# Kernel tuning notes

Measured on AMD Instinct MI355X. Metric: run time of the kernel, lower is better.

The kernel has to match this reference:

```python
import jax, jax.numpy as jnp
import numpy as np

EPS = 1e-5
ND, NDIS, NP, NG, NPW = 40000, 40000, 80000, 80000, 40000
D = 128


def gcn(x_src, src, dst, n_dst, W, b):
    # DGL GraphConv with norm='both': D_dst^{-1/2} A^T D_src^{-1/2} X W + b
    deg_out = jnp.maximum(jnp.zeros((x_src.shape[0],), x_src.dtype).at[src].add(1.0), 1.0)
    xs = x_src * (deg_out ** -0.5)[:, None]
    msg = jax.ops.segment_sum(xs[src], dst, num_segments=n_dst)
    deg_in = jnp.maximum(jnp.zeros((n_dst,), x_src.dtype).at[dst].add(1.0), 1.0)
    return (msg * (deg_in ** -0.5)[:, None]) @ W + b


def bn_prelu(v, gamma, beta, a):
    # BatchNorm1d (training-mode batch stats, biased var) then PReLU (scalar slope)
    mu = v.mean(0)
    var = v.var(0)
    y = gamma * (v - mu) / jnp.sqrt(var + EPS) + beta
    return jnp.where(y >= 0, y, a * y)


def sem_att(z, W1, b1, w2):
    # z: [N, K, D]; shared SemanticAttention across node types
    s = jnp.tanh(z @ W1 + b1) @ w2        # [N, K]
    beta = jax.nn.softmax(s.mean(0))       # [K]
    return jnp.einsum('k,nkd->nd', beta, z)


def setup_inputs():
    key = jax.random.key(0)
    ks = iter(jax.random.split(key, 40))
    f = lambda n: jax.random.normal(next(ks), (n, D), jnp.float32)
    inp = {'h_drug': f(ND), 'h_disease': f(NDIS), 'h_protein': f(NP),
           'h_gene': f(NG), 'h_pathway': f(NPW)}
    rels = {'dd': (ND, ND, 640000), 'ddi': (ND, NDIS, 640000), 'disdis': (NDIS, NDIS, 640000),
            'dp': (ND, NP, 640000), 'pp': (NP, NP, 1280000), 'pg': (NP, NG, 1280000),
            'gg': (NG, NG, 1280000), 'gpw': (NG, NPW, 1280000), 'pwpw': (NPW, NPW, 640000),
            'pwdis': (NPW, NDIS, 640000)}
    for name, (ns, nd, E) in rels.items():
        inp[name + '_src'] = jax.random.randint(next(ks), (E,), 0, ns)
        inp[name + '_dst'] = jax.random.randint(next(ks), (E,), 0, nd)
    inp['W_blocks'] = jax.random.normal(next(ks), (5, 3, D, D), jnp.float32) * 0.09
    inp['b_blocks'] = jnp.zeros((5, 3, D), jnp.float32)
    inp['bn_gamma'] = jnp.ones((5, D), jnp.float32)
    inp['bn_beta'] = jnp.zeros((5, D), jnp.float32)
    inp['prelu_a'] = jnp.full((5,), 0.25, jnp.float32)
    inp['attn_W1'] = jax.random.normal(next(ks), (D, D), jnp.float32) * 0.09
    inp['attn_b1'] = jnp.zeros((D,), jnp.float32)
    inp['attn_w2'] = jax.random.normal(next(ks), (D,), jnp.float32) * 0.09
    return inp


def reference(h_drug, h_disease, h_protein, h_gene, h_pathway,
              dd_src, dd_dst, ddi_src, ddi_dst, disdis_src, disdis_dst,
              dp_src, dp_dst, pp_src, pp_dst, pg_src, pg_dst,
              gg_src, gg_dst, gpw_src, gpw_dst, pwpw_src, pwpw_dst,
              pwdis_src, pwdis_dst,
              W_blocks, b_blocks, bn_gamma, bn_beta, prelu_a,
              attn_W1, attn_b1, attn_w2):
    act = lambda i, v: bn_prelu(v, bn_gamma[i], bn_beta[i], prelu_a[i])
    # block 0: drug_disease  (rels: drug_drug, drug_disease, disease_disease)
    d0 = act(0, gcn(h_drug, dd_src, dd_dst, ND, W_blocks[0, 0], b_blocks[0, 0]))
    dis0 = act(0, gcn(h_drug, ddi_src, ddi_dst, NDIS, W_blocks[0, 1], b_blocks[0, 1])
               + gcn(h_disease, disdis_src, disdis_dst, NDIS, W_blocks[0, 2], b_blocks[0, 2]))
    # block 1: drug_protein
    d1 = act(1, gcn(h_drug, dd_src, dd_dst, ND, W_blocks[1, 0], b_blocks[1, 0]))
    p1 = act(1, gcn(h_drug, dp_src, dp_dst, NP, W_blocks[1, 1], b_blocks[1, 1])
             + gcn(h_protein, pp_src, pp_dst, NP, W_blocks[1, 2], b_blocks[1, 2]))
    # block 2: protein_gene
    p2 = act(2, gcn(h_protein, pp_src, pp_dst, NP, W_blocks[2, 0], b_blocks[2, 0]))
    g2 = act(2, gcn(h_protein, pg_src, pg_dst, NG, W_blocks[2, 1], b_blocks[2, 1])
             + gcn(h_gene, gg_src, gg_dst, NG, W_blocks[2, 2], b_blocks[2, 2]))
    # block 3: gene_pathway
    g3 = act(3, gcn(h_gene, gg_src, gg_dst, NG, W_blocks[3, 0], b_blocks[3, 0]))
    pw3 = act(3, gcn(h_gene, gpw_src, gpw_dst, NPW, W_blocks[3, 1], b_blocks[3, 1])
              + gcn(h_pathway, pwpw_src, pwpw_dst, NPW, W_blocks[3, 2], b_blocks[3, 2]))
    # block 4: pathway_disease
    pw4 = act(4, gcn(h_pathway, pwpw_src, pwpw_dst, NPW, W_blocks[4, 0], b_blocks[4, 0]))
    dis4 = act(4, gcn(h_pathway, pwdis_src, pwdis_dst, NDIS, W_blocks[4, 1], b_blocks[4, 1])
               + gcn(h_disease, disdis_src, disdis_dst, NDIS, W_blocks[4, 2], b_blocks[4, 2]))
    att = lambda a, b: sem_att(jnp.stack([a, b], axis=1), attn_W1, attn_b1, attn_w2)
    return (att(d0, d1), att(dis0, dis4), att(p1, p2), att(g2, g3), att(pw3, pw4))
```

## Files before the change

kernel.cpp:

```cpp
#include <hip/hip_runtime.h>
#include <hip/hip_bf16.h>

#define D128 128

typedef __attribute__((ext_vector_type(8))) short bf16x8;
typedef __attribute__((ext_vector_type(4))) float f32x4;

__device__ inline unsigned short f2bf(float f) {
    unsigned u = __float_as_uint(f);
    u = u + 0x7fffu + ((u >> 16) & 1u);
    return (unsigned short)(u >> 16);
}
__device__ inline float bf2f(unsigned short h) {
    return __uint_as_float(((unsigned)h) << 16);
}
__device__ inline float fast_tanh(float x) {
    float e = __expf(2.f * x);
    return 1.f - 2.f * __builtin_amdgcn_rcpf(e + 1.f);
}

__device__ __forceinline__ void stage_w(const unsigned short* __restrict__ Wt,
                                        unsigned short* lw, int t)
{
    const uint4* srcW = (const uint4*)Wt;
    uint4* dstW = (uint4*)lw;
    for (int i = t; i < 2048; i += 256) {
        int row = i >> 4, sl = i & 15;
        dstW[row * 16 + (sl ^ (row & 7))] = srcW[i];
    }
}
__device__ __forceinline__ bf16x8 read_w(const unsigned short* lw, int row, int kt, int lq)
{
    int slot = (kt * 4 + lq) ^ (row & 7);
    return *(const bf16x8*)(lw + row * 128 + slot * 8);
}

__global__ __launch_bounds__(256) void xconv_scaled(
    const float* __restrict__ in, const int* __restrict__ degs,
    unsigned* __restrict__ out, int nrows)
{
    int t = threadIdx.x;
    int lane = t & 63, rr = t >> 6;
    int row = blockIdx.x * 4 + rr;
    if (row >= nrows) return;
    float sc = rsqrtf((float)max(degs[row], 1));
    float2 v = ((const float2*)(in + (size_t)row * 128))[lane];
    out[(size_t)row * 64 + lane] =
        (unsigned)f2bf(v.x * sc) | ((unsigned)f2bf(v.y * sc) << 16);
}

__global__ void wconv_t(const float* __restrict__ W_blocks, const float* __restrict__ W1,
                        unsigned short* __restrict__ wt)
{
    int m = blockIdx.x;
    const float* src = (m < 15) ? (W_blocks + (size_t)m * 16384) : W1;
    unsigned short* dst = wt + (size_t)m * 16384;
    for (int i = threadIdx.x; i < 16384; i += 256) {
        int n = i >> 7, k = i & 127;
        dst[i] = f2bf(src[k * 128 + n]);
    }
}

struct BuildArgs {
    const int* esrc[10]; const int* edst[10];
    int* histD; int* histS;
    int cumBlk[11]; int dstColBase[11]; int srcColBase[11]; int E[10];
};

__global__ __launch_bounds__(256) void part_count(BuildArgs A)
{
    __shared__ int hd[160], hs[320];
    int blk = blockIdx.x, t = threadIdx.x;
    int r = 0;
    while (r < 9 && blk >= A.cumBlk[r + 1]) r++;
    int blkInRel = blk - A.cumBlk[r];
    int nbD = A.dstColBase[r + 1] - A.dstColBase[r];
    int nbS = A.srcColBase[r + 1] - A.srcColBase[r];
    for (int i = t; i < nbD; i += 256) hd[i] = 0;
    for (int i = t; i < nbS; i += 256) hs[i] = 0;
    __syncthreads();
    int e0 = blkInRel * 16384;
    const int* sp = A.esrc[r];
    const int* dp = A.edst[r];
    int E = A.E[r];
#pragma unroll 4
    for (int j = 0; j < 64; j++) {
        int e = e0 + j * 256 + t;
        if (e < E) {
            atomicAdd(&hd[dp[e] >> 9], 1);
            atomicAdd(&hs[sp[e] >> 8], 1);
        }
    }
    __syncthreads();
    int cd = A.dstColBase[r], cs = A.srcColBase[r];
    for (int i = t; i < nbD; i += 256)
        A.histD[(size_t)(cd + i) * 80 + blkInRel] = hd[i];
    for (int i = t; i < nbS; i += 256)
        A.histS[(size_t)(cs + i) * 80 + blkInRel] = hs[i];
}

struct ScanArgs { int* hist; int* totals; int colBase[11]; int cumBlk[11]; };

__global__ __launch_bounds__(256) void col_scan(ScanArgs A)
{
    __shared__ int v[80];
    int col = blockIdx.x, t = threadIdx.x;
    int r = 0;
    while (r < 9 && col >= A.colBase[r + 1]) r++;
    int nblk = A.cumBlk[r + 1] - A.cumBlk[r];
    for (int i = t; i < nblk; i += 256) v[i] = A.hist[(size_t)col * 80 + i];
    __syncthreads();
    if (t == 0) {
        int run = 0;
        for (int i = 0; i < nblk; i++) { int c = v[i]; v[i] = run; run += c; }
        A.totals[col] = run;
    }
    __syncthreads();
    for (int i = t; i < nblk; i += 256) A.hist[(size_t)col * 80 + i] = v[i];
}

__global__ __launch_bounds__(256) void base_scan(const int* __restrict__ totals,
                                                 int* __restrict__ colbase, int n)
{
    __shared__ int v[2200];
    int t = threadIdx.x;
    for (int i = t; i < n; i += 256) v[i] = totals[i];
    __syncthreads();
    if (t == 0) {
        int run = 0;
        for (int i = 0; i < n; i++) { int c = v[i]; v[i] = run; run += c; }
        v[n] = run;
    }
    __syncthreads();
    for (int i = t; i <= n; i += 256) colbase[i] = v[i];
}

struct ScatArgs {
    const int* esrc[10]; const int* edst[10];
    const int* histD; const int* colbaseD;
    const int* histS; const int* colbaseS;
    int* epart; unsigned char* spart;
    int cumBlk[11]; int dstColBase[11]; int srcColBase[11]; int E[10];
};

__global__ __launch_bounds__(256) void scatter_all(ScatArgs A)
{
    __shared__ int hd[160], based[160], hs[320], bases[320];
    int blk = blockIdx.x, t = threadIdx.x;
    int r = 0;
    while (r < 9 && blk >= A.cumBlk[r + 1]) r++;
    int blkInRel = blk - A.cumBlk[r];
    int cd = A.dstColBase[r], cs = A.srcColBase[r];
    int nbD = A.dstColBase[r + 1] - cd;
    int nbS = A.srcColBase[r + 1] - cs;
    for (int i = t; i < nbD; i += 256) {
        based[i] = A.colbaseD[cd + i] + A.histD[(size_t)(cd + i) * 80 + blkInRel];
        hd[i] = 0;
    }
    for (int i = t; i < nbS; i += 256) {
        bases[i] = A.colbaseS[cs + i] + A.histS[(size_t)(cs + i) * 80 + blkInRel];
        hs[i] = 0;
    }
    __syncthreads();
    int e0 = blkInRel * 16384;
    const int* sp = A.esrc[r];
    const int* dp = A.edst[r];
    int E = A.E[r];
#pragma unroll 4
    for (int j = 0; j < 64; j++) {
        int e = e0 + j * 256 + t;
        if (e < E) {
            int s = sp[e], d = dp[e];
            int bd = d >> 9;
            int pd = atomicAdd(&hd[bd], 1);
            A.epart[based[bd] + pd] = (s & 0x1FFFF) | ((d & 511) << 17);
            int bs = s >> 8;
            int ps = atomicAdd(&hs[bs], 1);
            A.spart[(size_t)bases[bs] + ps] = (unsigned char)(s & 255);
        }
    }
}

struct FillArgs {
    const int* epart; const int* colbase;
    int* cursor; int* ebuf; int* oflow;
    int colBase[11];
    int cursorBase[10]; int ebufBase[10]; int cap[10]; int nd[10];
};

__global__ __launch_bounds__(256) void bucket_fill(FillArgs A)
{
    __shared__ int lcur[512];
    int col = blockIdx.x, t = threadIdx.x;
    int r = 0;
    while (r < 9 && col >= A.colBase[r + 1]) r++;
    int b = col - A.colBase[r];
    for (int i = t; i < 512; i += 256) lcur[i] = 0;
    __syncthreads();
    int start = A.colbase[col], end = A.colbase[col + 1];
    int cap = A.cap[r];
    int* eb = A.ebuf + (size_t)A.ebufBase[r];
    int* ofl = A.oflow + r * 8194;
    for (int i = start + t; i < end; i += 256) {
        int v = A.epart[i];
        int s = v & 0x1FFFF;
        int dlow = (v >> 17) & 511;
        int p = atomicAdd(&lcur[dlow], 1);
        if (p < cap) eb[(size_t)(b * 512 + dlow) * cap + p] = s;
        else {
            int q = atomicAdd(&ofl[0], 1);
            if (q < 4095) { ofl[2 + 2 * q] = b * 512 + dlow; ofl[3 + 2 * q] = s; }
        }
    }
    __syncthreads();
    for (int i = t; i < 512; i += 256) {
        int d = b * 512 + i;
        if (d < A.nd[r]) A.cursor[A.cursorBase[r] + d] = lcur[i];
    }
}

struct DegArgs {
    const unsigned char* spart; const int* colbase;
    int* degs;
    int colBase[11]; int degsBase[10]; int ns[10];
};

__global__ __launch_bounds__(256) void deg_count(DegArgs A)
{
    __shared__ int lc[256];
    int col = blockIdx.x, t = threadIdx.x;
    int r = 0;
    while (r < 9 && col >= A.colBase[r + 1]) r++;
    int b = col - A.colBase[r];
    lc[t] = 0;
    __syncthreads();
    int start = A.colbase[col], end = A.colbase[col + 1];
    for (int i = start + t; i < end; i += 256)
        atomicAdd(&lc[A.spart[i]], 1);
    __syncthreads();
    int s = b * 256 + t;
    if (s < A.ns[r]) A.degs[A.degsBase[r] + s] = lc[t];
}

__global__ __launch_bounds__(256) void gather_bf16(
    const unsigned* __restrict__ Xb,
    const int* __restrict__ cursor, const int* __restrict__ ebuf,
    const int* __restrict__ oflow, unsigned* __restrict__ aggb, int nd, int cap)
{
    int t = threadIdx.x;
    int lane = t & 63, r = t >> 6;
    int d = blockIdx.x * 4 + r;
    if (d >= nd) return;
    int cnt = cursor[d];
    int end = min(cnt, cap);
    const int* eb = ebuf + (size_t)d * cap;
    float a0 = 0.f, a1 = 0.f;
    int i = 0;
    for (; i + 4 <= end; i += 4) {
        int s0 = eb[i], s1 = eb[i + 1], s2 = eb[i + 2], s3 = eb[i + 3];
        unsigned x0 = Xb[(size_t)s0 * 64 + lane];
        unsigned x1 = Xb[(size_t)s1 * 64 + lane];
        unsigned x2 = Xb[(size_t)s2 * 64 + lane];
        unsigned x3 = Xb[(size_t)s3 * 64 + lane];
        a0 += bf2f((unsigned short)(x0 & 0xffff)) + bf2f((unsigned short)(x1 & 0xffff))
            + bf2f((unsigned short)(x2 & 0xffff)) + bf2f((unsigned short)(x3 & 0xffff));
        a1 += bf2f((unsigned short)(x0 >> 16)) + bf2f((unsigned short)(x1 >> 16))
            + bf2f((unsigned short)(x2 >> 16)) + bf2f((unsigned short)(x3 >> 16));
    }
    for (; i < end; i++) {
        int s0 = eb[i];
        unsigned x0 = Xb[(size_t)s0 * 64 + lane];
        a0 += bf2f((unsigned short)(x0 & 0xffff));
        a1 += bf2f((unsigned short)(x0 >> 16));
    }
    if (cnt > cap) {
        int n = min(oflow[0], 4095);
        for (int ii = 0; ii < n; ii++) {
            if (oflow[2 + 2 * ii] == d) {
                int s0 = oflow[3 + 2 * ii];
                unsigned x0 = Xb[(size_t)s0 * 64 + lane];
                a0 += bf2f((unsigned short)(x0 & 0xffff));
                a1 += bf2f((unsigned short)(x0 >> 16));
            }
        }
    }
    float sc = rsqrtf((float)max(cnt, 1));
    a0 *= sc; a1 *= sc;
    aggb[(size_t)d * 64 + lane] = (unsigned)f2bf(a0) | ((unsigned)f2bf(a1) << 16);
}

__device__ __forceinline__ void epi_store(
    f32x4* acc, unsigned short* __restrict__ Vb, int accum, int do_stats,
    float* ssum, float* ssq, int row0, int lr, int lq)
{
#pragma unroll
    for (int n = 0; n < 8; n++) {
        int col = n * 16 + lr;
        float s_ = 0.f, q_ = 0.f;
#pragma unroll
        for (int reg = 0; reg < 4; reg++) {
            int row = row0 + lq * 4 + reg;
            float v = acc[n][reg];
            unsigned short* vp = &Vb[(size_t)row * D128 + col];
            if (accum) v += bf2f(*vp);
            *vp = f2bf(v);
            s_ += v; q_ += v * v;
        }
        if (do_stats) {
            s_ += __shfl_xor(s_, 16); s_ += __shfl_xor(s_, 32);
            q_ += __shfl_xor(q_, 16); q_ += __shfl_xor(q_, 32);
            if (lq == 0) {
                atomicAdd(&ssum[col], s_);
                atomicAdd(&ssq[col], q_);
            }
        }
    }
}

__global__ __launch_bounds__(256) void gemm_mfma(
    const unsigned short* __restrict__ A, const unsigned short* __restrict__ Wt,
    unsigned short* __restrict__ Vb, int accum, int do_stats, float* __restrict__ statsraw)
{
    __shared__ unsigned short lw[16384];
    __shared__ float ssum[128], ssq[128];
    int t = threadIdx.x;
    int wave = t >> 6, lane = t & 63;
    int lr = lane & 15, lq = lane >> 4;
    int row0 = blockIdx.x * 64 + wave * 16;

    if (t < 128) { ssum[t] = 0.f; ssq[t] = 0.f; }
    stage_w(Wt, lw, t);
    __syncthreads();

    f32x4 acc[8];
#pragma unroll
    for (int n = 0; n < 8; n++) acc[n] = (f32x4)(0.f);

    const unsigned short* arow = A + (size_t)(row0 + lr) * 128 + lq * 8;
#pragma unroll
    for (int kt = 0; kt < 4; kt++) {
        bf16x8 af = *(const bf16x8*)(arow + kt * 32);
#pragma unroll
        for (int n = 0; n < 8; n++) {
            bf16x8 bfr = read_w(lw, n * 16 + lr, kt, lq);
            acc[n] = __builtin_amdgcn_mfma_f32_16x16x32_bf16(af, bfr, acc[n], 0, 0, 0);
        }
    }
    epi_store(acc, Vb, accum, do_stats, ssum, ssq, row0, lr, lq);
    if (do_stats) {
        __syncthreads();
        if (t < 128) atomicAdd(&statsraw[t], ssum[t]);
        else atomicAdd(&statsraw[t], ssq[t - 128]);
    }
}

__global__ __launch_bounds__(256) void gemm_mfma2(
    const unsigned short* __restrict__ A,
    const unsigned short* __restrict__ Wt0, const unsigned short* __restrict__ Wt1,
    unsigned short* __restrict__ V0b, unsigned short* __restrict__ V1b,
    int acc0f, int acc1f, int st0, int st1,
    float* __restrict__ sr0, float* __restrict__ sr1)
{
    __shared__ unsigned short lw0[16384], lw1[16384];
    __shared__ float ssum0[128], ssq0[128], ssum1[128], ssq1[128];
    int t = threadIdx.x;
    int wave = t >> 6, lane = t & 63;
    int lr = lane & 15, lq = lane >> 4;
    int row0 = blockIdx.x * 64 + wave * 16;

    if (t < 128) { ssum0[t] = 0.f; ssq0[t] = 0.f; ssum1[t] = 0.f; ssq1[t] = 0.f; }
    stage_w(Wt0, lw0, t);
    stage_w(Wt1, lw1, t);
    __syncthreads();

    f32x4 acc0[8], acc1[8];
#pragma unroll
    for (int n = 0; n < 8; n++) { acc0[n] = (f32x4)(0.f); acc1[n] = (f32x4)(0.f); }

    const unsigned short* arow = A + (size_t)(row0 + lr) * 128 + lq * 8;
#pragma unroll
    for (int kt = 0; kt < 4; kt++) {
        bf16x8 af = *(const bf16x8*)(arow + kt * 32);
#pragma unroll
        for (int n = 0; n < 8; n++) {
            int row = n * 16 + lr;
            bf16x8 b0 = read_w(lw0, row, kt, lq);
            bf16x8 b1 = read_w(lw1, row, kt, lq);
            acc0[n] = __builtin_amdgcn_mfma_f32_16x16x32_bf16(af, b0, acc0[n], 0, 0, 0);
            acc1[n] = __builtin_amdgcn_mfma_f32_16x16x32_bf16(af, b1, acc1[n], 0, 0, 0);
        }
    }
    epi_store(acc0, V0b, acc0f, st0, ssum0, ssq0, row0, lr, lq);
    epi_store(acc1, V1b, acc1f, st1, ssum1, ssq1, row0, lr, lq);
    __syncthreads();
    if (st0) {
        if (t < 128) atomicAdd(&sr0[t], ssum0[t]);
        else atomicAdd(&sr0[t], ssq0[t - 128]);
    }
    if (st1) {
        if (t < 128) atomicAdd(&sr1[t], ssum1[t]);
        else atomicAdd(&sr1[t], ssq1[t - 128]);
    }
}

struct FinArgs { int Ms[10]; };

__global__ void bn_finalize(const float* __restrict__ raw, float* __restrict__ fin, FinArgs fa)
{
    int tt = blockIdx.x;
    int c = threadIdx.x;
    float m = (float)fa.Ms[tt];
    float s = raw[tt * 256 + c], sq = raw[tt * 256 + 128 + c];
    float mu = s / m;
    float var = fmaxf(sq / m - mu * mu, 0.f);
    fin[tt * 256 + c] = mu;
    fin[tt * 256 + 128 + c] = rsqrtf(var + 1e-5f);
}

__global__ __launch_bounds__(256) void attn_t(
    const unsigned short* __restrict__ Vb, const float* __restrict__ raw, float Minv,
    const float* __restrict__ gam, const float* __restrict__ bet,
    const float* __restrict__ pa,
    const unsigned short* __restrict__ W1t, const float* __restrict__ b1,
    const float* __restrict__ w2, float* __restrict__ Sout)
{
    __shared__ float st[256];
    __shared__ float red[4];
    int t = threadIdx.x;
    if (t < 128) {
        float mu = raw[t] * Minv;
        float var = fmaxf(raw[128 + t] * Minv - mu * mu, 0.f);
        st[t] = mu;
        st[128 + t] = rsqrtf(var + 1e-5f);
    }
    __syncthreads();

    int wave = t >> 6, lane = t & 63;
    int lr = lane & 15, lq = lane >> 4;
    int row0 = blockIdx.x * 64 + wave * 16;
    float a = *pa;

    f32x4 acc[8];
#pragma unroll
    for (int n = 0; n < 8; n++) acc[n] = (f32x4)(0.f);

    const unsigned short* vrow = Vb + (size_t)(row0 + lr) * D128;
#pragma unroll
    for (int kt = 0; kt < 4; kt++) {
        int k0 = kt * 32 + lq * 8;
        bf16x8 vv = *(const bf16x8*)(vrow + k0);
        bf16x8 af;
#pragma unroll
        for (int jj = 0; jj < 8; jj++) {
            int cc = k0 + jj;
            float y = bf2f((unsigned short)vv[jj]);
            float yy = gam[cc] * (y - st[cc]) * st[128 + cc] + bet[cc];
            yy = yy >= 0.f ? yy : a * yy;
            af[jj] = (short)f2bf(yy);
        }
#pragma unroll
        for (int n = 0; n < 8; n++) {
            bf16x8 bfr = *(const bf16x8*)(W1t + (size_t)(n * 16 + lr) * 128 + k0);
            acc[n] = __builtin_amdgcn_mfma_f32_16x16x32_bf16(af, bfr, acc[n], 0, 0, 0);
        }
    }

    float thr = 0.f;
#pragma unroll
    for (int n = 0; n < 8; n++) {
        int col = n * 16 + lr;
        float bc = b1[col], wc = w2[col];
#pragma unroll
        for (int reg = 0; reg < 4; reg++)
            thr += fast_tanh(acc[n][reg] + bc) * wc;
    }
#pragma unroll
    for (int off = 1; off < 64; off <<= 1)
        thr += __shfl_xor(thr, off);
    if (lane == 0) red[wave] = thr;
    __syncthreads();
    if (t == 0) atomicAdd(Sout, red[0] + red[1] + red[2] + red[3]);
}

struct CombArgs {
    float* outp[5]; const unsigned short* va[5]; const unsigned short* vb[5];
    const float* stats; const float* gam; const float* bet; const float* pa; const float* S;
    int ta[5]; int tb[5]; int blka[5]; int blkb[5]; float invM[5]; int cum[6];
};

__global__ void combine_all(CombArgs D)
{
    int b = blockIdx.x, t = threadIdx.x;
    int p = 0;
    while (p < 4 && b >= D.cum[p + 1]) p++;
    size_t idx = (size_t)(b - D.cum[p]) * 256 + t;
    int c = (int)(idx & 127);
    float s0 = D.S[2 * p] * D.invM[p], s1 = D.S[2 * p + 1] * D.invM[p];
    float mx = fmaxf(s0, s1);
    float e0 = expf(s0 - mx), e1 = expf(s1 - mx);
    float inv = 1.f / (e0 + e1);
    float b0 = e0 * inv, b1w = e1 * inv;
    const float* sta = D.stats + D.ta[p] * 256;
    const float* stb = D.stats + D.tb[p] * 256;
    const float* ga = D.gam + D.blka[p] * 128;
    const float* ba = D.bet + D.blka[p] * 128;
    const float* gb = D.gam + D.blkb[p] * 128;
    const float* bb = D.bet + D.blkb[p] * 128;
    float aa = D.pa[D.blka[p]], ab = D.pa[D.blkb[p]];
    float va = bf2f(D.va[p][idx]);
    float vb = bf2f(D.vb[p][idx]);
    float ya = ga[c] * (va - sta[c]) * sta[128 + c] + ba[c];
    ya = ya >= 0.f ? ya : aa * ya;
    float yb = gb[c] * (vb - stb[c]) * stb[128 + c] + bb[c];
    yb = yb >= 0.f ? yb : ab * yb;
    D.outp[p][idx] = b0 * ya + b1w * yb;
}

extern "C" void kernel_launch(void* const* d_in, const int* in_sizes, int n_in,
                              void* d_out, int out_size, void* d_ws, size_t ws_size,
                              hipStream_t stream)
{
    const float* feats[5] = {
        (const float*)d_in[0], (const float*)d_in[1], (const float*)d_in[2],
        (const float*)d_in[3], (const float*)d_in[4]
    };
    const float* W_blocks = (const float*)d_in[25];
    const float* bn_gamma = (const float*)d_in[27];
    const float* bn_beta  = (const float*)d_in[28];
    const float* prelu_a  = (const float*)d_in[29];
    const float* attn_W1  = (const float*)d_in[30];
    const float* attn_b1  = (const float*)d_in[31];
    const float* attn_w2  = (const float*)d_in[32];
    float* out = (float*)d_out;

    unsigned* xbf  = (unsigned*)out;
    unsigned* aggb = (unsigned*)(out + 5120000);
    int*      ebuf = (int*)(out + 10240000);

    float* wsf = (float*)d_ws;
    unsigned short* wsvb = (unsigned short*)wsf;
    unsigned short* wtbf = (unsigned short*)(wsf + 35840000);
    int* degs     = (int*)(wsf + 35971072);
    int* cursor   = degs + 560000;
    int* oflow    = cursor + 560000;
    int* histD    = oflow + 81940;
    int* histS    = histD + 88160;
    int* colbaseD = histS + 175520;
    int* totalsD  = colbaseD + 1103;
    int* colbaseS = totalsD + 1102;
    int* totalsS  = colbaseS + 2195;
    int* epart    = totalsS + 2194;
    unsigned char* spart = (unsigned char*)(epart + 8960000);
    float* statsraw = (float*)(epart + 8960000 + 2240000);
    float* statsfin = statsraw + 2560;
    float* Ssum     = statsfin + 2560;
    size_t needed = ((size_t)((float*)(Ssum + 16) - wsf)) * 4;
    if (ws_size < needed) return;

    const int Mt[10]  = {40000, 40000, 40000, 40000, 80000, 80000, 80000, 80000, 40000, 40000};
    const int blk[10] = {0, 1, 0, 4, 1, 2, 2, 3, 3, 4};
    size_t offV[10];
    {
        size_t o = 0;
        for (int t = 0; t < 10; t++) { offV[t] = o; o += (size_t)Mt[t] * 128; }
    }
    unsigned short* Vb[10];
    for (int t = 0; t < 10; t++) Vb[t] = wsvb + offV[t];
    const size_t offT[5] = {0, 5120000, 10240000, 20480000, 30720000};

    const int relFeat[10] = {0, 0, 0, 1, 2, 2, 3, 3, 4, 4};
    const int relSrc[10]  = {5, 7, 11, 9, 13, 15, 17, 19, 21, 23};
    const int relNs[10]   = {40000, 40000, 40000, 40000, 80000, 80000, 80000, 80000, 40000, 40000};
    const int relNd[10]   = {40000, 40000, 80000, 40000, 80000, 80000, 80000, 40000, 40000, 40000};
    const int relE[10]    = {640000, 640000, 640000, 640000, 1280000,
                             1280000, 1280000, 1280000, 640000, 640000};
    const int relCap[10]  = {40, 40, 24, 40, 40, 40, 40, 56, 40, 40};
    const int cumBlk[11]  = {0, 40, 80, 120, 160, 239, 318, 397, 476, 516, 556};
    const int dstColBase[11] = {0, 79, 158, 315, 394, 551, 708, 865, 944, 1023, 1102};
    const int srcColBase[11] = {0, 157, 314, 471, 628, 941, 1254, 1567, 1880, 2037, 2194};
    const int degsBase[10]   = {0, 40000, 80000, 120000, 160000, 240000, 320000, 400000, 480000, 520000};
    const int cursorBase[10] = {0, 40000, 80000, 160000, 200000, 280000, 360000, 440000, 480000, 520000};
    const int ebufBase[10]   = {0, 1600000, 3200000, 5120000, 6720000, 9920000,
                                13120000, 16320000, 18560000, 20160000};

    struct GJob { int tid; int widx; int accum; int stats; };
    const int relNjob[10] = {2, 1, 1, 2, 2, 1, 2, 1, 2, 1};
    const GJob relJob[10][2] = {
        {{0,  0, 0, 1}, {1,  3, 0, 1}},
        {{2,  1, 0, 0}, {0,  0, 0, 0}},
        {{4,  4, 0, 0}, {0,  0, 0, 0}},
        {{2,  2, 1, 1}, {3, 14, 0, 0}},
        {{4,  5, 1, 1}, {5,  6, 0, 1}},
        {{6,  7, 0, 0}, {0,  0, 0, 0}},
        {{6,  8, 1, 1}, {7,  9, 0, 1}},
        {{8, 10, 0, 0}, {0,  0, 0, 0}},
        {{8, 11, 1, 1}, {9, 12, 0, 1}},
        {{3, 13, 1, 1}, {0,  0, 0, 0}},
    };
    const int doneCnt[10] = {2, 0, 0, 1, 2, 0, 2, 0, 2, 1};
    const int doneT[10][2] = {{0,1},{0,0},{0,0},{2,0},{4,5},{0,0},{6,7},{0,0},{8,9},{3,0}};

    wconv_t<<<16, 256, 0, stream>>>(W_blocks, attn_W1, wtbf);
    hipMemsetAsync(statsraw, 0, (2560 + 2560 + 16) * sizeof(float), stream);
    hipMemsetAsync(oflow, 0, (size_t)81940 * sizeof(int), stream);

    BuildArgs BA;
    ScanArgs  SAD, SAS;
    ScatArgs  CA;
    FillArgs  FA;
    DegArgs   DA;
    for (int r = 0; r < 10; r++) {
        BA.esrc[r] = (const int*)d_in[relSrc[r]];
        BA.edst[r] = (const int*)d_in[relSrc[r] + 1];
        BA.E[r] = relE[r];
        CA.esrc[r] = BA.esrc[r]; CA.edst[r] = BA.edst[r]; CA.E[r] = relE[r];
        FA.cursorBase[r] = cursorBase[r];
        FA.ebufBase[r] = ebufBase[r];
        FA.cap[r] = relCap[r];
        FA.nd[r] = relNd[r];
        DA.degsBase[r] = degsBase[r];
        DA.ns[r] = relNs[r];
    }
    for (int i = 0; i < 11; i++) {
        BA.cumBlk[i] = cumBlk[i]; BA.dstColBase[i] = dstColBase[i]; BA.srcColBase[i] = srcColBase[i];
        SAD.colBase[i] = dstColBase[i]; SAD.cumBlk[i] = cumBlk[i];
        SAS.colBase[i] = srcColBase[i]; SAS.cumBlk[i] = cumBlk[i];
        CA.cumBlk[i] = cumBlk[i]; CA.dstColBase[i] = dstColBase[i]; CA.srcColBase[i] = srcColBase[i];
        FA.colBase[i] = dstColBase[i];
        DA.colBase[i] = srcColBase[i];
    }
    BA.histD = histD; BA.histS = histS;
    SAD.hist = histD; SAD.totals = totalsD;
    SAS.hist = histS; SAS.totals = totalsS;
    CA.histD = histD; CA.colbaseD = colbaseD;
    CA.histS = histS; CA.colbaseS = colbaseS;
    CA.epart = epart; CA.spart = spart;
    FA.epart = epart; FA.colbase = colbaseD;
    FA.cursor = cursor; FA.ebuf = ebuf; FA.oflow = oflow;
    DA.spart = spart; DA.colbase = colbaseS; DA.degs = degs;

    part_count<<<556, 256, 0, stream>>>(BA);
    col_scan<<<1102, 256, 0, stream>>>(SAD);
    col_scan<<<2194, 256, 0, stream>>>(SAS);
    base_scan<<<1, 256, 0, stream>>>(totalsD, colbaseD, 1102);
    base_scan<<<1, 256, 0, stream>>>(totalsS, colbaseS, 2194);
    scatter_all<<<556, 256, 0, stream>>>(CA);
    bucket_fill<<<1102, 256, 0, stream>>>(FA);
    deg_count<<<2194, 256, 0, stream>>>(DA);

    for (int r = 0; r < 10; r++) {
        xconv_scaled<<<(relNs[r] + 3) / 4, 256, 0, stream>>>(
            feats[relFeat[r]], degs + degsBase[r], xbf, relNs[r]);
        gather_bf16<<<relNd[r] / 4, 256, 0, stream>>>(
            xbf, cursor + cursorBase[r],
            ebuf + (size_t)ebufBase[r], oflow + r * 8194, aggb, relNd[r], relCap[r]);
        if (relNjob[r] == 2) {
            const GJob& G0 = relJob[r][0];
            const GJob& G1 = relJob[r][1];
            gemm_mfma2<<<relNd[r] / 64, 256, 0, stream>>>(
                (const unsigned short*)aggb,
                wtbf + (size_t)G0.widx * 16384, wtbf + (size_t)G1.widx * 16384,
                Vb[G0.tid], Vb[G1.tid], G0.accum, G1.accum, G0.stats, G1.stats,
                statsraw + (size_t)G0.tid * 256, statsraw + (size_t)G1.tid * 256);
        } else {
            const GJob& G = relJob[r][0];
            gemm_mfma<<<relNd[r] / 64, 256, 0, stream>>>(
                (const unsigned short*)aggb, wtbf + (size_t)G.widx * 16384,
                Vb[G.tid], G.accum, G.stats, statsraw + (size_t)G.tid * 256);
        }
        for (int k = 0; k < doneCnt[r]; k++) {
            int t = doneT[r][k];
            attn_t<<<Mt[t] / 64, 256, 0, stream>>>(
                Vb[t], statsraw + (size_t)t * 256, 1.0f / Mt[t],
                bn_gamma + blk[t] * 128, bn_beta + blk[t] * 128, prelu_a + blk[t],
                wtbf + (size_t)15 * 16384, attn_b1, attn_w2, Ssum + t);
        }
    }

    FinArgs fa;
    for (int t = 0; t < 10; t++) fa.Ms[t] = Mt[t];
    bn_finalize<<<10, 128, 0, stream>>>(statsraw, statsfin, fa);

    CombArgs CD;
    CD.stats = statsfin; CD.gam = bn_gamma; CD.bet = bn_beta; CD.pa = prelu_a; CD.S = Ssum;
    CD.cum[0] = 0;
    for (int p = 0; p < 5; p++) {
        CD.outp[p] = out + offT[p];
        CD.va[p] = Vb[p * 2];
        CD.vb[p] = Vb[p * 2 + 1];
        CD.ta[p] = p * 2; CD.tb[p] = p * 2 + 1;
        CD.blka[p] = blk[p * 2]; CD.blkb[p] = blk[p * 2 + 1];
        CD.invM[p] = 1.0f / Mt[p * 2];
        CD.cum[p + 1] = CD.cum[p] + Mt[p * 2] / 2;
    }
    combine_all<<<CD.cum[5], 256, 0, stream>>>(CD);
}
```

Baseline: 1.614 ms.

## Stage scatter output in LDS to coalesce partitioned edge writes

The edge-partition scatter kernel now processes each 16K-edge block in four 4096-edge chunks. For each chunk it builds a local histogram and scans it, sorts the entries into LDS by bucket, and then writes them out contiguously, so global stores to epart/spart become mostly sequential runs instead of random single-element writes. This adds several barriers, two wave-level scans per chunk and about 40KB of LDS per block, which may reduce occupancy. It only affects the graph preprocessing stage.

```diff
diff --git a/kernel.cpp b/kernel.cpp
--- a/kernel.cpp
+++ b/kernel.cpp
@@ -33,6 +33,22 @@
 {
     int slot = (kt * 4 + lq) ^ (row & 7);
     return *(const bf16x8*)(lw + row * 128 + slot * 8);
+}
+
+__device__ __forceinline__ void wave_scan(const int* arr, int* ofs, int n, int lane)
+{
+    int k = (n + 63) >> 6;
+    int base = lane * k;
+    int sum = 0;
+    for (int i = 0; i < k; i++) { int idx = base + i; if (idx < n) sum += arr[idx]; }
+    int pre = sum;
+    for (int off = 1; off < 64; off <<= 1) {
+        int u = __shfl(pre, (lane - off) & 63);
+        if (lane >= off) pre += u;
+    }
+    int run = pre - sum;
+    for (int i = 0; i < k; i++) { int idx = base + i; if (idx < n) { ofs[idx] = run; run += arr[idx]; } }
+    if (lane == 63) ofs[n] = run;
 }
 
 __global__ __launch_bounds__(256) void xconv_scaled(
@@ -145,7 +161,13 @@
 
 __global__ __launch_bounds__(256) void scatter_all(ScatArgs A)
 {
-    __shared__ int hd[160], based[160], hs[320], bases[320];
+    __shared__ int stageE[4096];
+    __shared__ unsigned short bidS[4096];
+    __shared__ unsigned char bidE[4096];
+    __shared__ unsigned char stageS[4096];
+    __shared__ int gbaseD[160], gcurD[160], lhistD[160], lofsD[161];
+    __shared__ int gbaseS[320], gcurS[320], lhistS[320], lofsS[321];
+
     int blk = blockIdx.x, t = threadIdx.x;
     int r = 0;
     while (r < 9 && blk >= A.cumBlk[r + 1]) r++;
@@ -154,30 +176,73 @@
     int nbD = A.dstColBase[r + 1] - cd;
     int nbS = A.srcColBase[r + 1] - cs;
     for (int i = t; i < nbD; i += 256) {
-        based[i] = A.colbaseD[cd + i] + A.histD[(size_t)(cd + i) * 80 + blkInRel];
-        hd[i] = 0;
+        gbaseD[i] = A.colbaseD[cd + i] + A.histD[(size_t)(cd + i) * 80 + blkInRel];
+        gcurD[i] = 0;
     }
     for (int i = t; i < nbS; i += 256) {
-        bases[i] = A.colbaseS[cs + i] + A.histS[(size_t)(cs + i) * 80 + blkInRel];
-        hs[i] = 0;
-    }
-    __syncthreads();
-    int e0 = blkInRel * 16384;
+        gbaseS[i] = A.colbaseS[cs + i] + A.histS[(size_t)(cs + i) * 80 + blkInRel];
+        gcurS[i] = 0;
+    }
     const int* sp = A.esrc[r];
     const int* dp = A.edst[r];
     int E = A.E[r];
-#pragma unroll 4
-    for (int j = 0; j < 64; j++) {
-        int e = e0 + j * 256 + t;
-        if (e < E) {
-            int s = sp[e], d = dp[e];
-            int bd = d >> 9;
-            int pd = atomicAdd(&hd[bd], 1);
-            A.epart[based[bd] + pd] = (s & 0x1FFFF) | ((d & 511) << 17);
-            int bs = s >> 8;
-            int ps = atomicAdd(&hs[bs], 1);
-            A.spart[(size_t)bases[bs] + ps] = (unsigned char)(s & 255);
-        }
+    int blkbase = blkInRel * 16384;
+
+    for (int c = 0; c < 4; c++) {
+        int e0 = blkbase + c * 4096;
+        int sv[16], dv[16];
+#pragma unroll
+        for (int j = 0; j < 16; j++) {
+            int e = e0 + j * 256 + t;
+            sv[j] = (e < E) ? sp[e] : -1;
+            dv[j] = (e < E) ? dp[e] : 0;
+        }
+        for (int i = t; i < nbD; i += 256) lhistD[i] = 0;
+        for (int i = t; i < nbS; i += 256) lhistS[i] = 0;
+        __syncthreads();
+#pragma unroll
+        for (int j = 0; j < 16; j++) {
+            if (sv[j] >= 0) {
+                atomicAdd(&lhistD[dv[j] >> 9], 1);
+                atomicAdd(&lhistS[sv[j] >> 8], 1);
+            }
+        }
+        __syncthreads();
+        if (t < 64) wave_scan(lhistD, lofsD, nbD, t);
+        else if (t < 128) wave_scan(lhistS, lofsS, nbS, t - 64);
+        __syncthreads();
+        for (int i = t; i < nbD; i += 256) lhistD[i] = 0;
+        for (int i = t; i < nbS; i += 256) lhistS[i] = 0;
+        __syncthreads();
+#pragma unroll
+        for (int j = 0; j < 16; j++) {
+            if (sv[j] >= 0) {
+                int bd = dv[j] >> 9;
+                int p = atomicAdd(&lhistD[bd], 1);
+                int ix = lofsD[bd] + p;
+                stageE[ix] = (sv[j] & 0x1FFFF) | ((dv[j] & 511) << 17);
+                bidE[ix] = (unsigned char)bd;
+                int bs = sv[j] >> 8;
+                int q = atomicAdd(&lhistS[bs], 1);
+                int iy = lofsS[bs] + q;
+                stageS[iy] = (unsigned char)(sv[j] & 255);
+                bidS[iy] = (unsigned short)bs;
+            }
+        }
+        __syncthreads();
+        int cntv = lofsD[nbD];
+        for (int i = t; i < cntv; i += 256) {
+            int b = bidE[i];
+            A.epart[gbaseD[b] + gcurD[b] + i - lofsD[b]] = stageE[i];
+        }
+        for (int i = t; i < cntv; i += 256) {
+            int b = bidS[i];
+            A.spart[(size_t)gbaseS[b] + gcurS[b] + i - lofsS[b]] = stageS[i];
+        }
+        __syncthreads();
+        for (int i = t; i < nbD; i += 256) gcurD[i] += lofsD[i + 1] - lofsD[i];
+        for (int i = t; i < nbS; i += 256) gcurS[i] += lofsS[i + 1] - lofsS[i];
+        __syncthreads();
     }
 }
 
```

Result: faster. 1.548 ms (-4.1%).
